# Optimization experiments

Measured on AMD Instinct MI355X. Metric: run time of the kernel, lower is better.

## Reference

```python
import jax, jax.numpy as jnp
import numpy as np

B, H, W, C = 4, 128, 128, 256
D_MODEL, NH = 512, 8
DH = D_MODEL // NH  # 64


def setup_inputs() -> dict:
    key = jax.random.key(0)
    ks = jax.random.split(key, 5)
    s = lambda fan_in: 1.0 / np.sqrt(fan_in)
    return {
        "x": jax.random.normal(ks[0], (B, H, W, C), jnp.float32),
        "Wq": jax.random.normal(ks[1], (C, D_MODEL), jnp.float32) * s(C),
        "bq": jnp.zeros((D_MODEL,), jnp.float32),
        "Wk": jax.random.normal(ks[2], (C, D_MODEL), jnp.float32) * s(C),
        "bk": jnp.zeros((D_MODEL,), jnp.float32),
        "Wv": jax.random.normal(ks[3], (C, D_MODEL), jnp.float32) * s(C),
        "bv": jnp.zeros((D_MODEL,), jnp.float32),
        "Wo": jax.random.normal(ks[4], (D_MODEL, C), jnp.float32) * s(D_MODEL),
        "bo": jnp.zeros((C,), jnp.float32),
    }


def reference(x, Wq, bq, Wk, bk, Wv, bv, Wo, bo):
    # Axial multi-head attention along axis 1 (H), W axis is batched.
    b, h, w, _ = x.shape
    q = (x @ Wq + bq).reshape(b, h, w, NH, DH) * (DH ** -0.5)
    k = (x @ Wk + bk).reshape(b, h, w, NH, DH)
    v = (x @ Wv + bv).reshape(b, h, w, NH, DH)
    # scores over the H axis: [B, Nh, W, H, H]
    scores = jnp.einsum("bxwnd,bywnd->bnwxy", q, k)
    probs = jax.nn.softmax(scores, axis=-1)
    # [B, H, W, Nh, DH] -> [B, H, W, d_model]
    out = jnp.einsum("bnwxy,bywnd->bxwnd", probs, v).reshape(b, h, w, D_MODEL)
    # Wo projection; original combines to [B,W,H,C] then permutes back to [B,H,W,C],
    # which is equivalent to applying Wo directly here. Dropout is identity at inference.
    return out @ Wo + bo
```

## Files before the change

kernel.cpp:

```cpp
#include <hip/hip_runtime.h>

typedef unsigned short u16;
typedef __attribute__((ext_vector_type(8))) short bf16x8;
typedef __attribute__((ext_vector_type(8))) unsigned short u16x8;
typedef __attribute__((ext_vector_type(4))) unsigned u32x4;
typedef __attribute__((ext_vector_type(4))) float f32x4;

#define DEVI static __device__ __forceinline__

DEVI u16 f2b(float f) {
  unsigned u = __builtin_bit_cast(unsigned, f);
  return (u16)((u + 0x7FFFu + ((u >> 16) & 1u)) >> 16);
}

DEVI unsigned cvtpk(float a, float b) {
  unsigned r;
  asm("v_cvt_pk_bf16_f32 %0, %1, %2" : "=v"(r) : "v"(a), "v"(b));
  return r;
}

DEVI void gload_lds16(const void* g, void* l) {
  __builtin_amdgcn_global_load_lds(
      (const __attribute__((address_space(1))) unsigned int*)g,
      (__attribute__((address_space(3))) unsigned int*)l, 16, 0, 0);
}


__global__ __launch_bounds__(256) void prep_x(const float* __restrict__ x, u16* __restrict__ xb) {
  const int n8 = 65536 * 256 / 8;
  int i = blockIdx.x * blockDim.x + threadIdx.x;
  for (; i < n8; i += gridDim.x * blockDim.x) {
    const float4* p = (const float4*)x + (size_t)i * 2;
    float4 a = p[0], b = p[1];
    u16x8 r;
    r[0] = f2b(a.x); r[1] = f2b(a.y); r[2] = f2b(a.z); r[3] = f2b(a.w);
    r[4] = f2b(b.x); r[5] = f2b(b.y); r[6] = f2b(b.z); r[7] = f2b(b.w);
    *(u16x8*)(xb + (size_t)i * 8) = r;
  }
}

__global__ __launch_bounds__(256) void prep_w(
    const float* __restrict__ Wq, const float* __restrict__ Wk,
    const float* __restrict__ Wv, const float* __restrict__ Wo,
    const float* __restrict__ bq, const float* __restrict__ bk, const float* __restrict__ bv,
    u16* __restrict__ wqkvT, u16* __restrict__ woT, float* __restrict__ bqkv) {
  const int NW1 = 1536 * 256, NW2 = 256 * 512;
  const int total = NW1 + NW2 + 1536;
  int i = blockIdx.x * blockDim.x + threadIdx.x;
  for (; i < total; i += gridDim.x * blockDim.x) {
    if (i < NW1) {
      int nn = i >> 8, kk = i & 255;
      float v;
      if (nn < 512)       v = Wq[kk * 512 + nn] * 0.125f;
      else if (nn < 1024) v = Wk[kk * 512 + (nn - 512)];
      else                v = Wv[kk * 512 + (nn - 1024)];
      wqkvT[i] = f2b(v);
    } else if (i < NW1 + NW2) {
      int j = i - NW1;
      int nn = j >> 9, kk = j & 511;
      woT[j] = f2b(Wo[kk * 256 + nn]);
    } else {
      int j = i - NW1 - NW2;
      bqkv[j] = (j < 512) ? bq[j] * 0.125f : (j < 1024 ? bk[j - 512] : bv[j - 1024]);
    }
  }
}


__global__ __launch_bounds__(256) void gemm128p(
    const u16* __restrict__ A, const u16* __restrict__ Bt,
    const float* __restrict__ bias, u16* __restrict__ Cg) {
  constexpr int KK = 256, NT = 4;
  __shared__ u16 smem[16384];
  const int tid = threadIdx.x;
  const int lane = tid & 63, wid = tid >> 6;
  const int nTn = 12;
  const int qx = gridDim.x >> 3;
  const int wg = (blockIdx.x & 7) * qx + (blockIdx.x >> 3);
  const long m0 = (long)(wg / nTn) * 128;
  const long n0 = (long)(wg % nTn) * 128;
  const int wr = wid >> 1, wc = wid & 1;
  const int hi = lane >> 4, lo = lane & 15;
  const u16* Ab = A + m0 * KK;
  const u16* Bb = Bt + n0 * KK;
  const int srow_ = tid >> 3;
  const int schunk = tid & 7;

  f32x4 acc[4][4];
#pragma unroll
  for (int mi = 0; mi < 4; ++mi)
#pragma unroll
    for (int ni = 0; ni < 4; ++ni) acc[mi][ni] = f32x4{0.f, 0.f, 0.f, 0.f};

#pragma unroll
  for (int t = 0; t < NT; ++t) {
    const int kt = t * 64;
#pragma unroll
    for (int j = 0; j < 4; ++j) {
      int row = j * 32 + srow_;
      int colE = (schunk ^ (row & 7)) << 3;
      gload_lds16(Ab + (long)row * KK + kt + colE, &smem[(j * 256 + tid) * 8]);
    }
#pragma unroll
    for (int j = 0; j < 4; ++j) {
      int row = j * 32 + srow_;
      int colE = (schunk ^ (row & 7)) << 3;
      gload_lds16(Bb + (long)row * KK + kt + colE, &smem[8192 + (j * 256 + tid) * 8]);
    }
    asm volatile("s_waitcnt vmcnt(0)" ::: "memory");
    __builtin_amdgcn_sched_barrier(0);
    __builtin_amdgcn_s_barrier();
    const u16* aB = smem;
    const u16* bB = smem + 8192;
#pragma unroll
    for (int ks = 0; ks < 2; ++ks) {
      const int slot = ((hi + ks * 4) ^ (lo & 7)) << 3;
      bf16x8 af[4], bfr[4];
#pragma unroll
      for (int mi = 0; mi < 4; ++mi)
        af[mi] = *(const bf16x8*)&aB[(wr * 64 + mi * 16 + lo) * 64 + slot];
#pragma unroll
      for (int ni = 0; ni < 4; ++ni)
        bfr[ni] = *(const bf16x8*)&bB[(wc * 64 + ni * 16 + lo) * 64 + slot];
#pragma unroll
      for (int mi = 0; mi < 4; ++mi)
#pragma unroll
        for (int ni = 0; ni < 4; ++ni)
          acc[mi][ni] = __builtin_amdgcn_mfma_f32_16x16x32_bf16(af[mi], bfr[ni], acc[mi][ni], 0, 0, 0);
    }
    __builtin_amdgcn_sched_barrier(0);
    __builtin_amdgcn_s_barrier();
  }

  float bb[4];
#pragma unroll
  for (int ni = 0; ni < 4; ++ni) bb[ni] = bias[n0 + wc * 64 + ni * 16 + lo];

#pragma unroll
  for (int mi = 0; mi < 4; ++mi)
#pragma unroll
    for (int ni = 0; ni < 4; ++ni) {
#pragma unroll
      for (int j = 0; j < 4; ++j) {
        int row = wr * 64 + mi * 16 + hi * 4 + j;
        int chunk = (wc * 8 + ni * 2 + (lo >> 3)) ^ ((row >> 2) & 7);
        smem[row * 128 + chunk * 8 + (lo & 7)] = f2b(acc[mi][ni][j] + bb[ni]);
      }
    }
  __syncthreads();
#pragma unroll
  for (int it = 0; it < 8; ++it) {
    int idx = it * 256 + tid;
    int row = idx >> 4, c = idx & 15;
    int cs = c ^ ((row >> 2) & 7);
    long m = m0 + row;
    int col = (int)n0 + c * 8;
    int b_ = (int)(m >> 14), yw = (int)m & 16383;
    int y = yw >> 7, w = yw & 127;
    int t = col >> 9, h = (col >> 6) & 7, dh = col & 63;
    size_t dst = ((((size_t)(b_ * 128 + w) * 8 + h) * 3 + t) * 128 + y) * 64 + dh;
    *(u16x8*)(Cg + dst) = *(const u16x8*)&smem[row * 128 + cs * 8];
  }
}


template <int KK>
__global__ __launch_bounds__(1024) void gemm256(
    const u16* __restrict__ A, const u16* __restrict__ Bt,
    const float* __restrict__ bias, void* __restrict__ Cv, int N) {
  constexpr int NT = KK / 64;
  __shared__ u16 smem[65536];
  const int tid = threadIdx.x;
  const int lane = tid & 63, wid = tid >> 6;
  const int nTn = N >> 8;
  const int qx = gridDim.x >> 3;
  const int wg = (blockIdx.x & 7) * qx + (blockIdx.x >> 3);
  const long m0 = (long)(wg / nTn) * 256;
  const long n0 = (long)(wg % nTn) * 256;
  const int wr = wid >> 2, wc = wid & 3;
  const int hi = lane >> 4, lo = lane & 15;
  const u16* Ab = A + m0 * KK;
  const u16* Bb = Bt + n0 * KK;
  const int srow_ = tid >> 3;
  const int schunk = tid & 7;

  f32x4 acc[4][4];
#pragma unroll
  for (int mi = 0; mi < 4; ++mi)
#pragma unroll
    for (int ni = 0; ni < 4; ++ni) acc[mi][ni] = f32x4{0.f, 0.f, 0.f, 0.f};

  auto stage = [&](int t) {
    u16* base = &smem[(t & 1) * 32768];
    const int kt = t * 64;
#pragma unroll
    for (int j = 0; j < 2; ++j) {
      int row = j * 128 + srow_;
      int colE = (schunk ^ (row & 7)) << 3;
      gload_lds16(Ab + (long)row * KK + kt + colE, &base[(j * 1024 + tid) * 8]);
    }
#pragma unroll
    for (int j = 0; j < 2; ++j) {
      int row = j * 128 + srow_;
      int colE = (schunk ^ (row & 7)) << 3;
      gload_lds16(Bb + (long)row * KK + kt + colE, &base[16384 + (j * 1024 + tid) * 8]);
    }
  };

  stage(0);
#pragma unroll
  for (int t = 0; t < NT; ++t) {
    if (t + 1 < NT) {
      stage(t + 1);
      asm volatile("s_waitcnt vmcnt(4)" ::: "memory");
    } else {
      asm volatile("s_waitcnt vmcnt(0)" ::: "memory");
    }
    __builtin_amdgcn_sched_barrier(0);
    __builtin_amdgcn_s_barrier();
    const u16* aB = &smem[(t & 1) * 32768];
    const u16* bB = aB + 16384;
#pragma unroll
    for (int ks = 0; ks < 2; ++ks) {
      const int slot = ((hi + ks * 4) ^ (lo & 7)) << 3;
      bf16x8 af[4], bfr[4];
#pragma unroll
      for (int mi = 0; mi < 4; ++mi)
        af[mi] = *(const bf16x8*)&aB[(wr * 64 + mi * 16 + lo) * 64 + slot];
#pragma unroll
      for (int ni = 0; ni < 4; ++ni)
        bfr[ni] = *(const bf16x8*)&bB[(wc * 64 + ni * 16 + lo) * 64 + slot];
#pragma unroll
      for (int mi = 0; mi < 4; ++mi)
#pragma unroll
        for (int ni = 0; ni < 4; ++ni)
          acc[mi][ni] = __builtin_amdgcn_mfma_f32_16x16x32_bf16(af[mi], bfr[ni], acc[mi][ni], 0, 0, 0);
    }
    __builtin_amdgcn_sched_barrier(0);
    __builtin_amdgcn_s_barrier();
  }

  float bb[4];
#pragma unroll
  for (int ni = 0; ni < 4; ++ni) bb[ni] = bias[n0 + wc * 64 + ni * 16 + lo];

  float* Cg = (float*)Cv;
#pragma unroll
  for (int mi = 0; mi < 4; ++mi)
#pragma unroll
    for (int ni = 0; ni < 4; ++ni) {
      long cg = n0 + wc * 64 + ni * 16 + lo;
#pragma unroll
      for (int j = 0; j < 4; ++j)
        Cg[(m0 + wr * 64 + mi * 16 + hi * 4 + j) * N + cg] = acc[mi][ni][j] + bb[ni];
    }
}


__global__ __launch_bounds__(256, 5) void attn_axial(const u16* __restrict__ qkv,
                                                     u16* __restrict__ ao) {
  __shared__ u16 smem[16384];
  u16* kld = smem;
  u16* vt  = smem + 8192;

  const int g = blockIdx.x;
  const int n = g & 7, w = (g >> 3) & 127, b = g >> 10;
  const int tid = threadIdx.x, lane = tid & 63, wid = tid >> 6;
  const size_t pq = (((size_t)(b * 128 + w) * 8 + n) * 3) * 8192;
  const u16* Qp = qkv + pq;
  const u16* Kp = qkv + pq + 8192;
  const u16* Vp = qkv + pq + 16384;
  const int hi = lane >> 4, lo = lane & 15;

  {
    const int kr0 = tid >> 3, kc = tid & 7;
#pragma unroll
    for (int i = 0; i < 4; ++i) {
      const int row = i * 32 + kr0;
      const int srcC = (kc ^ (row & 7)) << 3;
      gload_lds16(Kp + row * 64 + srcC, &kld[(i * 256 + tid) * 8]);
    }
  }

  const int vyp = (tid & 63) * 2;
  const u16* vg = Vp + vyp * 64 + wid * 16;
  u16x8 va0 = *(const u16x8*)vg;
  u16x8 va1 = *(const u16x8*)(vg + 8);
  u16x8 vc0 = *(const u16x8*)(vg + 64);
  u16x8 vc1 = *(const u16x8*)(vg + 72);

  bf16x8 qf[2][2];
#pragma unroll
  for (int cg = 0; cg < 2; ++cg)
#pragma unroll
    for (int ks = 0; ks < 2; ++ks)
      qf[cg][ks] = *(const bf16x8*)(Qp + (wid * 32 + cg * 16 + lo) * 64 + hi * 8 + ks * 32);

  {
    unsigned* vt32 = (unsigned*)vt;
    const int cch = vyp >> 3;
    const int cw = (vyp >> 1) & 3;
#pragma unroll
    for (int e = 0; e < 8; ++e) {
      const int d0 = wid * 16 + e, d1 = wid * 16 + 8 + e;
      const int c0s = (cch & 8) | ((cch & 7) ^ (d0 & 7));
      const int c1s = (cch & 8) | ((cch & 7) ^ (d1 & 7));
      vt32[d0 * 64 + c0s * 4 + cw] = (unsigned)va0[e] | ((unsigned)vc0[e] << 16);
      vt32[d1 * 64 + c1s * 4 + cw] = (unsigned)va1[e] | ((unsigned)vc1[e] << 16);
    }
  }

  __syncthreads();

  f32x4 s2[2][8];
#pragma unroll
  for (int cg = 0; cg < 2; ++cg)
#pragma unroll
    for (int ni = 0; ni < 8; ++ni) s2[cg][ni] = f32x4{0.f, 0.f, 0.f, 0.f};
  __builtin_amdgcn_s_setprio(1);
#pragma unroll
  for (int ks = 0; ks < 2; ++ks)
#pragma unroll
    for (int ni = 0; ni < 8; ++ni) {
      const int kr = ni * 16 + lo;
      bf16x8 kf = *(const bf16x8*)&kld[kr * 64 + (((hi + ks * 4) ^ (kr & 7)) << 3)];
      s2[0][ni] = __builtin_amdgcn_mfma_f32_16x16x32_bf16(kf, qf[0][ks], s2[0][ni], 0, 0, 0);
      s2[1][ni] = __builtin_amdgcn_mfma_f32_16x16x32_bf16(kf, qf[1][ks], s2[1][ni], 0, 0, 0);
    }
  __builtin_amdgcn_s_setprio(0);

  unsigned setA[2][4][2], setB[2][4][2];
#pragma unroll
  for (int cg = 0; cg < 2; ++cg) {
    float mx = s2[cg][0][0];
#pragma unroll
    for (int ni = 0; ni < 8; ++ni)
#pragma unroll
      for (int j = 0; j < 4; ++j) mx = fmaxf(mx, s2[cg][ni][j]);
    mx = fmaxf(mx, __shfl_xor(mx, 16, 64));
    mx = fmaxf(mx, __shfl_xor(mx, 32, 64));
    float sum = 0.f;
#pragma unroll
    for (int ni = 0; ni < 8; ++ni)
#pragma unroll
      for (int j = 0; j < 4; ++j) {
        float e = exp2f((s2[cg][ni][j] - mx) * 1.44269504f);
        s2[cg][ni][j] = e;
        sum += e;
      }
    sum += __shfl_xor(sum, 16, 64);
    sum += __shfl_xor(sum, 32, 64);
    const float r = 1.f / sum;

    unsigned pkE[4][2], pkO[4][2];
#pragma unroll
    for (int o = 0; o < 4; ++o) {
      pkE[o][0] = cvtpk(s2[cg][2 * o][0] * r, s2[cg][2 * o][1] * r);
      pkE[o][1] = cvtpk(s2[cg][2 * o][2] * r, s2[cg][2 * o][3] * r);
      pkO[o][0] = cvtpk(s2[cg][2 * o + 1][0] * r, s2[cg][2 * o + 1][1] * r);
      pkO[o][1] = cvtpk(s2[cg][2 * o + 1][2] * r, s2[cg][2 * o + 1][3] * r);
    }
    const bool lowHi = (hi < 2);
    unsigned keepR[4][2], gotR[4][2];
#pragma unroll
    for (int o = 0; o < 4; ++o)
#pragma unroll
      for (int e = 0; e < 2; ++e) {
        unsigned snd = lowHi ? pkO[o][e] : pkE[o][e];
        keepR[o][e] = lowHi ? pkE[o][e] : pkO[o][e];
        gotR[o][e] = __shfl_xor(snd, 32, 64);
      }
    const bool fwdGot = (hi == 0) || (hi == 3);
    unsigned recv2[4][2];
#pragma unroll
    for (int o = 0; o < 4; ++o)
#pragma unroll
      for (int e = 0; e < 2; ++e) {
        unsigned snd = fwdGot ? gotR[o][e] : keepR[o][e];
        recv2[o][e] = __shfl_xor(snd, 16, 64);
      }
#pragma unroll
    for (int o = 0; o < 4; ++o)
#pragma unroll
      for (int e = 0; e < 2; ++e) {
        setA[cg][o][e] = (hi & 1) ? recv2[o][e] : (hi == 0 ? keepR[o][e] : gotR[o][e]);
        setB[cg][o][e] = (hi & 1) ? (hi == 1 ? gotR[o][e] : keepR[o][e]) : recv2[o][e];
      }
  }

  f32x4 o2[2][4];
#pragma unroll
  for (int cg = 0; cg < 2; ++cg)
#pragma unroll
    for (int ni = 0; ni < 4; ++ni) o2[cg][ni] = f32x4{0.f, 0.f, 0.f, 0.f};
  __builtin_amdgcn_s_setprio(1);
#pragma unroll
  for (int ks = 0; ks < 4; ++ks) {
    const int cch = hi + ks * 4;
    bf16x8 pa[2];
#pragma unroll
    for (int cg = 0; cg < 2; ++cg) {
      u32x4 t;
      t[0] = setA[cg][ks][0]; t[1] = setA[cg][ks][1];
      t[2] = setB[cg][ks][0]; t[3] = setB[cg][ks][1];
      pa[cg] = __builtin_bit_cast(bf16x8, t);
    }
#pragma unroll
    for (int ni = 0; ni < 4; ++ni) {
      const int vr = ni * 16 + lo;
      const int cs = (cch & 8) | ((cch & 7) ^ (vr & 7));
      bf16x8 vf = *(const bf16x8*)&vt[vr * 128 + cs * 8];
      o2[0][ni] = __builtin_amdgcn_mfma_f32_16x16x32_bf16(pa[0], vf, o2[0][ni], 0, 0, 0);
      o2[1][ni] = __builtin_amdgcn_mfma_f32_16x16x32_bf16(pa[1], vf, o2[1][ni], 0, 0, 0);
    }
  }
  __builtin_amdgcn_s_setprio(0);

#pragma unroll
  for (int cg = 0; cg < 2; ++cg)
#pragma unroll
    for (int j = 0; j < 4; ++j) {
      const int q = wid * 32 + cg * 16 + hi * 4 + j;
      const size_t obase = ((size_t)(b * 16384 + q * 128 + w)) * 512 + (size_t)n * 64;
#pragma unroll
      for (int ni = 0; ni < 4; ++ni)
        ao[obase + ni * 16 + lo] = f2b(o2[cg][ni][j]);
    }
}


extern "C" void kernel_launch(void* const* d_in, const int* in_sizes, int n_in,
                              void* d_out, int out_size, void* d_ws, size_t ws_size,
                              hipStream_t stream) {
  (void)in_sizes; (void)n_in; (void)out_size; (void)ws_size;
  const float* x  = (const float*)d_in[0];
  const float* Wq = (const float*)d_in[1];
  const float* bq = (const float*)d_in[2];
  const float* Wk = (const float*)d_in[3];
  const float* bk = (const float*)d_in[4];
  const float* Wv = (const float*)d_in[5];
  const float* bv = (const float*)d_in[6];
  const float* Wo = (const float*)d_in[7];
  const float* bo = (const float*)d_in[8];
  float* out = (float*)d_out;

  char* ws = (char*)d_ws;
  const size_t MiB = (size_t)1 << 20;
  u16* qkv   = (u16*)ws;
  u16* xb    = (u16*)(ws + 192 * MiB);
  u16* wqkvT = (u16*)(ws + 224 * MiB);
  u16* woT   = wqkvT + 1536 * 256;
  float* bqkv = (float*)(woT + 256 * 512);

  prep_x<<<2048, 256, 0, stream>>>(x, xb);
  prep_w<<<512, 256, 0, stream>>>(Wq, Wk, Wv, Wo, bq, bk, bv, wqkvT, woT, bqkv);

  gemm128p<<<6144, 256, 0, stream>>>(xb, wqkvT, bqkv, qkv);
  attn_axial<<<4096, 256, 0, stream>>>(qkv, (u16*)out);
  gemm256<512><<<256, 1024, 0, stream>>>((const u16*)out, woT, bo, out, 256);
}
```

Measured before the change: 212.3 us.

## Tile QKV projection by (batch, column) so each block writes contiguous head slabs

The QKV projection GEMM now gives each 128-row tile the 128 H positions of one (b, w) column instead of 128 consecutive rows. It reads A with a stride of 32768 elements (one H step) rather than contiguously. The qkv buffer layout also changes from [b,w,head,t] to [b,w,t,head], so each block's output tile lands in contiguous 8192-element slabs, and the attention kernel's pointer math is updated to match. The goal is simpler, more coalesced epilogue stores and better locality for the attention kernel, at the cost of strided A-row loads in the GEMM.

```diff
diff --git a/kernel.cpp b/kernel.cpp
--- a/kernel.cpp
+++ b/kernel.cpp
@@ -77,14 +77,17 @@
   const int nTn = 12;
   const int qx = gridDim.x >> 3;
   const int wg = (blockIdx.x & 7) * qx + (blockIdx.x >> 3);
-  const long m0 = (long)(wg / nTn) * 128;
-  const long n0 = (long)(wg % nTn) * 128;
+  const int ct = wg / nTn;
+  const int n0 = (wg % nTn) * 128;
+  const long abase = (long)ct == 0 ? 0 : 0;
+  const int b_ = ct >> 7, w_ = ct & 127;
+  const long aoff = ((long)b_ * 16384 + w_) * 256;
   const int wr = wid >> 1, wc = wid & 1;
   const int hi = lane >> 4, lo = lane & 15;
-  const u16* Ab = A + m0 * KK;
-  const u16* Bb = Bt + n0 * KK;
+  const u16* Bb = Bt + (long)n0 * KK;
   const int srow_ = tid >> 3;
   const int schunk = tid & 7;
+  (void)abase;
 
   f32x4 acc[4][4];
 #pragma unroll
@@ -99,7 +102,7 @@
     for (int j = 0; j < 4; ++j) {
       int row = j * 32 + srow_;
       int colE = (schunk ^ (row & 7)) << 3;
-      gload_lds16(Ab + (long)row * KK + kt + colE, &smem[(j * 256 + tid) * 8]);
+      gload_lds16(A + aoff + (long)row * 32768 + kt + colE, &smem[(j * 256 + tid) * 8]);
     }
 #pragma unroll
     for (int j = 0; j < 4; ++j) {
@@ -148,18 +151,16 @@
       }
     }
   __syncthreads();
+  const size_t pbase = (size_t)ct * 24 * 8192;
 #pragma unroll
   for (int it = 0; it < 8; ++it) {
     int idx = it * 256 + tid;
-    int row = idx >> 4, c = idx & 15;
-    int cs = c ^ ((row >> 2) & 7);
-    long m = m0 + row;
-    int col = (int)n0 + c * 8;
-    int b_ = (int)(m >> 14), yw = (int)m & 16383;
-    int y = yw >> 7, w = yw & 127;
+    int y = idx >> 4, c = idx & 15;
+    int cs = c ^ ((y >> 2) & 7);
+    int col = n0 + c * 8;
     int t = col >> 9, h = (col >> 6) & 7, dh = col & 63;
-    size_t dst = ((((size_t)(b_ * 128 + w) * 8 + h) * 3 + t) * 128 + y) * 64 + dh;
-    *(u16x8*)(Cg + dst) = *(const u16x8*)&smem[row * 128 + cs * 8];
+    size_t dst = pbase + (size_t)(t * 8 + h) * 8192 + y * 64 + dh;
+    *(u16x8*)(Cg + dst) = *(const u16x8*)&smem[y * 128 + cs * 8];
   }
 }
 
@@ -266,10 +267,10 @@
   const int g = blockIdx.x;
   const int n = g & 7, w = (g >> 3) & 127, b = g >> 10;
   const int tid = threadIdx.x, lane = tid & 63, wid = tid >> 6;
-  const size_t pq = (((size_t)(b * 128 + w) * 8 + n) * 3) * 8192;
-  const u16* Qp = qkv + pq;
-  const u16* Kp = qkv + pq + 8192;
-  const u16* Vp = qkv + pq + 16384;
+  const size_t pb = (size_t)(b * 128 + w) * 24 * 8192;
+  const u16* Qp = qkv + pb + (size_t)n * 8192;
+  const u16* Kp = qkv + pb + (size_t)(8 + n) * 8192;
+  const u16* Vp = qkv + pb + (size_t)(16 + n) * 8192;
   const int hi = lane >> 4, lo = lane & 15;
 
   {
```

Result: faster. 201.6 us (-5.1%).
